# Performance work log

Measured on AMD Instinct MI355X. Metric: run time of the kernel, lower is better.

Reference implementation:

```python
import jax, jax.numpy as jnp
import numpy as np
import math

T, B, C, H, W = 1, 64, 512, 8, 8
E, NH, MEM, FF = 512, 8, 32, 2048
HD = E // NH            # 64 per-head channels
TOT = HD * H * W        # 4096 = flattened per-head dim (channels x spatial)


def conv2d(x, w, b):
    # NCHW conv with 'same' padding, matching torch.nn.Conv2d(padding='same')
    y = jax.lax.conv_general_dilated(x, w, (1, 1), 'SAME',
                                     dimension_numbers=('NCHW', 'OIHW', 'NCHW'))
    return y + b[None, :, None, None]


def layernorm(x, w, b, eps=1e-5):
    # LayerNorm over (C,H,W) with elementwise affine, matching nn.LayerNorm((C,H,W))
    m = jnp.mean(x, axis=(1, 2, 3), keepdims=True)
    v = jnp.var(x, axis=(1, 2, 3), keepdims=True)
    return (x - m) * jax.lax.rsqrt(v + eps) * w[None] + b[None]


def setup_inputs() -> dict:
    key = jax.random.key(0)
    ks = jax.random.split(key, 16)
    s = 0.02
    inp = {
        'input': jax.random.normal(ks[0], (T, B, C, H, W), jnp.float32),
        'attn_mask': jax.random.randint(ks[1], (B * NH, T, MEM), 0, 2) == 1,
        'concat_k': jax.random.normal(ks[2], (B, MEM, NH, TOT), jnp.float32),
        'concat_v': jax.random.normal(ks[3], (B, MEM, NH, TOT), jnp.float32),
        'proj_w': jax.random.normal(ks[4], (3 * E, C, 3, 3), jnp.float32) * s,
        'proj_b': jnp.zeros((3 * E,), jnp.float32),
        'out_w': jax.random.normal(ks[5], (E, E, 3, 3), jnp.float32) * s,
        'out_b': jnp.zeros((E,), jnp.float32),
        'lin1_w': jax.random.normal(ks[6], (FF, E, 3, 3), jnp.float32) * s,
        'lin1_b': jnp.zeros((FF,), jnp.float32),
        'lin2_w': jax.random.normal(ks[7], (E, FF, 3, 3), jnp.float32) * s,
        'lin2_b': jnp.zeros((E,), jnp.float32),
        'n1_w': jnp.ones((E, H, W), jnp.float32),
        'n1_b': jnp.zeros((E, H, W), jnp.float32),
        'n2_w': jnp.ones((E, H, W), jnp.float32),
        'n2_b': jnp.zeros((E, H, W), jnp.float32),
        'pos_w': jax.random.normal(ks[8], (MEM, H * W * E), jnp.float32) * s,
        'pos_b': jax.random.uniform(ks[9], (MEM, NH), jnp.float32, -0.1, 0.1),
    }
    return inp


def reference(input, attn_mask, concat_k, concat_v, proj_w, proj_b, out_w, out_b,
              lin1_w, lin1_b, lin2_w, lin2_b, n1_w, n1_b, n2_w, n2_b, pos_w, pos_b):
    x = input.reshape(T * B, C, H, W)
    kqv = conv2d(x, proj_w, proj_b)                      # [B, 3E, H, W]
    k0, q0, v0 = kqv[:, :E], kqv[:, E:2 * E], kqv[:, 2 * E:]

    def split_heads(t):  # [T*B,E,H,W] -> [B*NH, T, TOT]
        return t.reshape(T, B * NH, HD, H, W).transpose(1, 0, 2, 3, 4).reshape(B * NH, T, TOT)

    k, q, v = split_heads(k0), split_heads(q0), split_heads(v0)
    q = q / math.sqrt(TOT)

    def mem_pre(c):  # [B,MEM,NH,TOT] -> [B*NH, MEM-1, TOT]
        return c[:, 1:].transpose(1, 0, 2, 3).reshape(MEM - 1, B * NH, TOT).transpose(1, 0, 2)

    k = jnp.concatenate([mem_pre(concat_k), k], axis=1)  # [B*NH, MEM, TOT]
    v = jnp.concatenate([mem_pre(concat_v), v], axis=1)

    # learned relative-position bias on keys and logits
    pw = jnp.broadcast_to(pos_w[:, None, :], (MEM, B, NH * TOT)).reshape(MEM, B * NH, TOT).transpose(1, 0, 2)
    pb = jnp.broadcast_to(pos_b[:, None, :], (MEM, B, NH)).reshape(MEM, B * NH).transpose(1, 0)
    k = k + pw

    mask = jnp.where(attn_mask, -jnp.inf, 0.0).astype(q.dtype)
    mask = mask.at[:, :, -1].set(5.0)                    # current step always attendable (+5 bias)
    logits = mask + jnp.einsum('bqd,bkd->bqk', q, k) + pb[:, None, :]
    w_attn = jax.nn.softmax(logits, axis=-1)             # [B*NH, T, MEM]
    attn = jnp.einsum('bqk,bkd->bqd', w_attn, v)         # [B*NH, T, TOT]
    attn = attn.transpose(1, 0, 2).reshape(B, E, H, W)

    out = conv2d(attn, out_w, out_b)
    ret_k = k.transpose(1, 0, 2).reshape(MEM, B, NH, TOT).transpose(1, 0, 2, 3)
    ret_v = v.transpose(1, 0, 2).reshape(MEM, B, NH, TOT).transpose(1, 0, 2, 3)

    # norm_first=False path
    out = out + x[:, :E]
    out = layernorm(out, n1_w, n1_b)
    ff = conv2d(jax.nn.relu(conv2d(out, lin1_w, lin1_b)), lin2_w, lin2_b)
    out = layernorm(out + ff, n2_w, n2_b)
    return (out[None], ret_k, ret_v)
```

## Files before the change

kernel.cpp:

```cpp
#include <hip/hip_runtime.h>
#include <hip/hip_bf16.h>
#include <stdint.h>

typedef __attribute__((ext_vector_type(8))) short bf16x8;
typedef __attribute__((ext_vector_type(4))) float f32x4;

static __device__ __forceinline__ unsigned short f2bf(float f) {
  union { float f; unsigned int u; } v; v.f = f;
  unsigned int u = v.u;
  return (unsigned short)((u + 0x7FFFu + ((u >> 16) & 1u)) >> 16);
}

static __device__ __forceinline__ void gld16(const void* g, void* l) {
  __builtin_amdgcn_global_load_lds(
      (const __attribute__((address_space(1))) unsigned int*)g,
      (__attribute__((address_space(3))) unsigned int*)l, 16, 0, 0);
}

__global__ __launch_bounds__(256) void k_zero(uint4* __restrict__ p, int n) {
  int i = blockIdx.x * 256 + threadIdx.x;
  if (i < n) p[i] = make_uint4(0u, 0u, 0u, 0u);
}

__global__ __launch_bounds__(256) void k_wcvt(const float* __restrict__ in,
                                              unsigned short* __restrict__ out, int C) {
  int o = blockIdx.x, c0 = blockIdx.y << 9;
  int t = threadIdx.x;
  __shared__ float l[4608];
  const float* src = in + ((size_t)o * C + c0) * 9;
  for (int j = t; j < 4608; j += 256) l[j] = src[j];
  __syncthreads();
  unsigned short* dst = out + (size_t)o * 9 * C;
#pragma unroll
  for (int j = 0; j < 18; ++j) {
    int f = t * 18 + j;
    int tap = f >> 9, c = f & 511;
    dst[(size_t)tap * C + c0 + c] = f2bf(l[c * 9 + tap]);
  }
}

__global__ __launch_bounds__(256) void k_x2pad(const float* __restrict__ x,
                                               unsigned short* __restrict__ xp) {
  int b = blockIdx.x >> 3, c0 = (blockIdx.x & 7) << 6;
  int t = threadIdx.x;
  __shared__ float l[64][65];
  int cr = t >> 2, p0 = (t & 3) << 4;
  const float* src = x + ((size_t)b * 512 + c0 + cr) * 64 + p0;
#pragma unroll
  for (int j = 0; j < 4; ++j) {
    float4 v = *(const float4*)(src + j * 4);
    l[cr][p0 + j * 4 + 0] = v.x; l[cr][p0 + j * 4 + 1] = v.y;
    l[cr][p0 + j * 4 + 2] = v.z; l[cr][p0 + j * 4 + 3] = v.w;
  }
  __syncthreads();
  int pix = t >> 2, cc0 = (t & 3) << 4;
  size_t prow = (size_t)b * 100 + 11 + (pix >> 3) * 10 + (pix & 7);
  unsigned short pk[16];
#pragma unroll
  for (int j = 0; j < 16; ++j) pk[j] = f2bf(l[cc0 + j][pix]);
  *(uint4*)(xp + prow * 512 + c0 + cc0) = *(const uint4*)pk;
  *(uint4*)(xp + prow * 512 + c0 + cc0 + 8) = *(const uint4*)(pk + 8);
}

template <int EPI>
__global__ __launch_bounds__(256, 2) void k_gemm9(
    const unsigned short* __restrict__ Wt, int ldK,
    const unsigned short* __restrict__ Xp, int C, int tlog,
    int kiter, const float* __restrict__ bias,
    void* __restrict__ outv, int Cout, size_t zstride) {
  __shared__ unsigned short lds[2][2][8192];
  int t = threadIdx.x, lane = t & 63, wid = t >> 6;
  int O0 = blockIdx.x << 7, M0 = blockIdx.y << 7;
  int kbase = blockIdx.z * kiter;
  int srow = lane >> 3, skg = (lane & 7) << 3;

  int wrow[4], pbv[4];
#pragma unroll
  for (int i = 0; i < 4; ++i) {
    int rl = wid * 8 + i * 32 + srow;
    wrow[i] = O0 + rl;
    int m = M0 + rl, b = m >> 6, pix = m & 63;
    pbv[i] = b * 100 + (pix >> 3) * 10 + (pix & 7);
  }

  f32x4 acc[4][4];
#pragma unroll
  for (int i = 0; i < 4; ++i)
#pragma unroll
    for (int j = 0; j < 4; ++j) acc[i][j] = (f32x4){0.f, 0.f, 0.f, 0.f};

  auto stage = [&](int buf, int kt) {
    int gk = kbase + kt;
    int tap = gk >> tlog;
    int c0 = (gk - (tap << tlog)) << 6;
    int toff = tap + 7 * ((tap * 11) >> 5);
#pragma unroll
    for (int i = 0; i < 4; ++i) {
      gld16(Wt + (size_t)wrow[i] * ldK + (gk << 6) + skg,
            &lds[buf][0][(wid * 8 + i * 32) * 64]);
      gld16(Xp + (size_t)(pbv[i] + toff) * C + c0 + skg,
            &lds[buf][1][(wid * 8 + i * 32) * 64]);
    }
  };

  int wr = wid >> 1, wc = wid & 1;
  int frow = lane & 15, fkb = (lane >> 4) << 3;

  auto compute = [&](int buf) {
    const unsigned short* Wl = &lds[buf][0][0];
    const unsigned short* Xl = &lds[buf][1][0];
#pragma unroll
    for (int kk = 0; kk < 2; ++kk) {
      bf16x8 af[4], bfv[4];
#pragma unroll
      for (int f = 0; f < 4; ++f) {
        af[f]  = *(const bf16x8*)(Wl + ((wr * 64 + f * 16 + frow) << 6) + kk * 32 + fkb);
        bfv[f] = *(const bf16x8*)(Xl + ((wc * 64 + f * 16 + frow) << 6) + kk * 32 + fkb);
      }
#pragma unroll
      for (int fi = 0; fi < 4; ++fi)
#pragma unroll
        for (int fj = 0; fj < 4; ++fj)
          acc[fi][fj] = __builtin_amdgcn_mfma_f32_16x16x32_bf16(af[fi], bfv[fj], acc[fi][fj], 0, 0, 0);
    }
  };

  stage(0, 0);
  __syncthreads();
  for (int kt = 0; kt < kiter; ++kt) {
    int cur = kt & 1;
    if (kt + 1 < kiter) stage(cur ^ 1, kt + 1);
    compute(cur);
    __syncthreads();
  }

  int ob = O0 + wr * 64, mb = M0 + wc * 64;
  int r0 = (lane >> 4) << 2, cm = lane & 15;
  if (EPI == 4) {
    unsigned short* outp = (unsigned short*)outv;
#pragma unroll
    for (int fi = 0; fi < 4; ++fi) {
      int oo = ob + fi * 16 + r0;
      float4 bv = *(const float4*)(bias + oo);
#pragma unroll
      for (int fj = 0; fj < 4; ++fj) {
        int mm = mb + fj * 16 + cm;
        int bb = mm >> 6, pix = mm & 63;
        size_t prow = (size_t)bb * 100 + 11 + (pix >> 3) * 10 + (pix & 7);
        unsigned short pk[4];
        pk[0] = f2bf(fmaxf(acc[fi][fj][0] + bv.x, 0.f));
        pk[1] = f2bf(fmaxf(acc[fi][fj][1] + bv.y, 0.f));
        pk[2] = f2bf(fmaxf(acc[fi][fj][2] + bv.z, 0.f));
        pk[3] = f2bf(fmaxf(acc[fi][fj][3] + bv.w, 0.f));
        *(ushort4*)(outp + prow * Cout + oo) = *(const ushort4*)pk;
      }
    }
  } else {
    float* out = (float*)outv + (size_t)blockIdx.z * zstride;
#pragma unroll
    for (int fi = 0; fi < 4; ++fi) {
#pragma unroll
      for (int fj = 0; fj < 4; ++fj) {
        int mm = mb + fj * 16 + cm;
        int bb = mm >> 6, pix = mm & 63;
#pragma unroll
        for (int r = 0; r < 4; ++r) {
          int oo = ob + fi * 16 + r0 + r;
          float v = acc[fi][fj][r];
          if (EPI == 0) v += bias[oo];
          out[((size_t)bb * Cout + oo) * 64 + pix] = v;
        }
      }
    }
  }
}

__global__ __launch_bounds__(256) void k_attnK(
    const float* __restrict__ kqv, const float* __restrict__ ck,
    const float* __restrict__ pw, const float* __restrict__ pb,
    float* __restrict__ rk, float* __restrict__ logits) {
  int idx = blockIdx.x;
  int h = idx & 7, m = (idx >> 3) & 31, b = idx >> 8;
  int t = threadIdx.x, lane = t & 63, wid = t >> 6;
  int i0 = t << 4;
  int hd = i0 >> 6, pix = i0 & 63;

  const float* src = (m < 31)
      ? (ck + (((size_t)(b * 32 + m + 1) * 8 + h) << 12) + i0)
      : (kqv + ((size_t)(b * 1536 + h * 64 + hd) << 6) + pix);
  const float* qs = kqv + ((size_t)(b * 1536 + 512 + h * 64 + hd) << 6) + pix;
  const float* pws = pw + ((size_t)m << 15) + (h << 12) + i0;
  float* dst = rk + (((size_t)(b * 32 + m) * 8 + h) << 12) + i0;

  float part = 0.f;
#pragma unroll
  for (int j = 0; j < 4; ++j) {
    float4 a = *(const float4*)(src + j * 4);
    float4 p = *(const float4*)(pws + j * 4);
    float4 q = *(const float4*)(qs + j * 4);
    float4 kk;
    kk.x = a.x + p.x; kk.y = a.y + p.y; kk.z = a.z + p.z; kk.w = a.w + p.w;
    *(float4*)(dst + j * 4) = kk;
    part += 0.015625f * (q.x * kk.x + q.y * kk.y + q.z * kk.z + q.w * kk.w);
  }
#pragma unroll
  for (int s = 32; s; s >>= 1) part += __shfl_xor(part, s);
  __shared__ float red[4];
  if (lane == 0) red[wid] = part;
  __syncthreads();
  if (t == 0)
    logits[((b << 3) + h) * 32 + m] = red[0] + red[1] + red[2] + red[3] + pb[m * 8 + h];
}

__global__ __launch_bounds__(256) void k_attnV(
    const float* __restrict__ kqv, const int* __restrict__ mask,
    const float* __restrict__ cv, const float* __restrict__ logits,
    float* __restrict__ rv, float* __restrict__ attnb) {
  int bh = blockIdx.x, b = bh >> 3, h = bh & 7;
  int t = threadIdx.x;
  int d = (blockIdx.y << 10) + (t << 2);
  int hd = d >> 6, pix = d & 63;

  float lg[32];
#pragma unroll
  for (int j = 0; j < 8; ++j) {
    float4 v = *(const float4*)(logits + bh * 32 + j * 4);
    lg[j * 4 + 0] = v.x; lg[j * 4 + 1] = v.y; lg[j * 4 + 2] = v.z; lg[j * 4 + 3] = v.w;
  }
  float mx = -INFINITY;
#pragma unroll
  for (int m = 0; m < 32; ++m) {
    if (m == 31) lg[m] += 5.0f;
    else if (mask[bh * 32 + m] != 0) lg[m] = -INFINITY;
    mx = fmaxf(mx, lg[m]);
  }
  float sm = 0.f;
#pragma unroll
  for (int m = 0; m < 32; ++m) { lg[m] = __expf(lg[m] - mx); sm += lg[m]; }
  float rs = 1.f / sm;

  float4 acc = make_float4(0.f, 0.f, 0.f, 0.f);
  for (int m = 0; m < 32; ++m) {
    const float* src = (m < 31)
        ? (cv + (((size_t)(b * 32 + m + 1) * 8 + h) << 12) + d)
        : (kqv + ((size_t)(b * 1536 + 1024 + h * 64 + hd) << 6) + pix);
    float4 v = *(const float4*)src;
    *(float4*)(rv + (((size_t)(b * 32 + m) * 8 + h) << 12) + d) = v;
    float wm = lg[m] * rs;
    acc.x += wm * v.x; acc.y += wm * v.y; acc.z += wm * v.z; acc.w += wm * v.w;
  }
  *(float4*)(attnb + ((size_t)(b * 512 + h * 64 + hd) << 6) + pix) = acc;
}

__global__ __launch_bounds__(256) void k_lnfuse(
    const float* __restrict__ a, const float* __restrict__ b,
    const float* __restrict__ resid, const float* __restrict__ bias,
    const float* __restrict__ w, const float* __restrict__ beta,
    float* __restrict__ out) {
  int bb = blockIdx.x, t = threadIdx.x, lane = t & 63, wid = t >> 6;
  size_t base = (size_t)bb << 15;
  float s = 0.f, sq = 0.f;
  for (int i = t * 4; i < 32768; i += 1024) {
    float4 va = *(const float4*)(a + base + i);
    float4 vb = *(const float4*)(b + base + i);
    float4 vr = *(const float4*)(resid + base + i);
    float bs = bias[i >> 6];
    float x0 = va.x + vb.x + vr.x + bs, x1 = va.y + vb.y + vr.y + bs;
    float x2 = va.z + vb.z + vr.z + bs, x3 = va.w + vb.w + vr.w + bs;
    s += x0 + x1 + x2 + x3;
    sq += x0 * x0 + x1 * x1 + x2 * x2 + x3 * x3;
  }
#pragma unroll
  for (int k = 32; k; k >>= 1) { s += __shfl_xor(s, k); sq += __shfl_xor(sq, k); }
  __shared__ float rsm[4], rqm[4];
  if (lane == 0) { rsm[wid] = s; rqm[wid] = sq; }
  __syncthreads();
  s = rsm[0] + rsm[1] + rsm[2] + rsm[3];
  sq = rqm[0] + rqm[1] + rqm[2] + rqm[3];
  float mean = s * (1.f / 32768.f);
  float var = sq * (1.f / 32768.f) - mean * mean;
  float rinv = rsqrtf(var + 1e-5f);
  for (int i = t * 4; i < 32768; i += 1024) {
    float4 va = *(const float4*)(a + base + i);
    float4 vb = *(const float4*)(b + base + i);
    float4 vr = *(const float4*)(resid + base + i);
    float bs = bias[i >> 6];
    float4 vw = *(const float4*)(w + i);
    float4 vt = *(const float4*)(beta + i);
    float4 r;
    r.x = (va.x + vb.x + vr.x + bs - mean) * rinv * vw.x + vt.x;
    r.y = (va.y + vb.y + vr.y + bs - mean) * rinv * vw.y + vt.y;
    r.z = (va.z + vb.z + vr.z + bs - mean) * rinv * vw.z + vt.z;
    r.w = (va.w + vb.w + vr.w + bs - mean) * rinv * vw.w + vt.w;
    *(float4*)(out + base + i) = r;
  }
}

extern "C" void kernel_launch(void* const* d_in, const int* in_sizes, int n_in,
                              void* d_out, int out_size, void* d_ws, size_t ws_size,
                              hipStream_t stream) {
  const float* x     = (const float*)d_in[0];
  const int*   mask  = (const int*)d_in[1];
  const float* ck    = (const float*)d_in[2];
  const float* cv    = (const float*)d_in[3];
  const float* projw = (const float*)d_in[4];
  const float* projb = (const float*)d_in[5];
  const float* outw  = (const float*)d_in[6];
  const float* outb  = (const float*)d_in[7];
  const float* l1w   = (const float*)d_in[8];
  const float* l1b   = (const float*)d_in[9];
  const float* l2w   = (const float*)d_in[10];
  const float* l2b   = (const float*)d_in[11];
  const float* n1w   = (const float*)d_in[12];
  const float* n1b   = (const float*)d_in[13];
  const float* n2w   = (const float*)d_in[14];
  const float* n2b   = (const float*)d_in[15];
  const float* posw  = (const float*)d_in[16];
  const float* posb  = (const float*)d_in[17];

  char* ws = (char*)d_ws;
  unsigned short* wbP   = (unsigned short*)(ws);
  unsigned short* wbO   = (unsigned short*)(ws + 14155776);
  unsigned short* wbL1  = (unsigned short*)(ws + 18874368);
  unsigned short* wbL2  = (unsigned short*)(ws + 37748736);
  unsigned short* xpadI = (unsigned short*)(ws + 56623104);
  unsigned short* apad  = (unsigned short*)(ws + 63176704);
  unsigned short* l1pad = (unsigned short*)(ws + 69730304);
  unsigned short* ffpad = (unsigned short*)(ws + 76283904);
  float* kqv    = (float*)(ws + 102498304);
  float* logits = (float*)(ws + 127664128);
  float* res_a  = (float*)(ws + 127729664);
  float* res_b  = (float*)(ws + 136118272);
  float* ln1    = (float*)(ws + 144506880);
  float* attnb  = (float*)(ws + 152895488);

  float* out0 = (float*)d_out;
  float* rk = out0 + 2097152;
  float* rv = rk + 67108864;

  k_zero<<<11200, 256, 0, stream>>>((uint4*)(ws + 56623104), 2867200);

  k_wcvt<<<dim3(1536, 1), 256, 0, stream>>>(projw, wbP, 512);
  k_wcvt<<<dim3(512, 1), 256, 0, stream>>>(outw, wbO, 512);
  k_wcvt<<<dim3(2048, 1), 256, 0, stream>>>(l1w, wbL1, 512);
  k_wcvt<<<dim3(512, 4), 256, 0, stream>>>(l2w, wbL2, 2048);

  k_x2pad<<<512, 256, 0, stream>>>(x, xpadI);

  k_gemm9<0><<<dim3(12, 32, 1), 256, 0, stream>>>(wbP, 4608, xpadI, 512, 3, 72, projb, kqv, 1536, 0);

  k_attnK<<<16384, 256, 0, stream>>>(kqv, ck, posw, posb, rk, logits);
  k_attnV<<<dim3(512, 4), 256, 0, stream>>>(kqv, mask, cv, logits, rv, attnb);
  k_x2pad<<<512, 256, 0, stream>>>(attnb, apad);

  k_gemm9<3><<<dim3(4, 32, 2), 256, 0, stream>>>(wbO, 4608, apad, 512, 3, 36, nullptr, res_a, 512, 2097152);
  k_lnfuse<<<64, 256, 0, stream>>>(res_a, res_b, x, outb, n1w, n1b, ln1);
  k_x2pad<<<512, 256, 0, stream>>>(ln1, l1pad);

  k_gemm9<4><<<dim3(16, 32, 1), 256, 0, stream>>>(wbL1, 4608, l1pad, 512, 3, 72, l1b, ffpad, 2048, 0);

  k_gemm9<3><<<dim3(4, 32, 2), 256, 0, stream>>>(wbL2, 18432, ffpad, 2048, 5, 144, nullptr, res_a, 512, 2097152);
  k_lnfuse<<<64, 256, 0, stream>>>(res_a, res_b, ln1, l2b, n2w, n2b, out0);
}
```

Before: 891.4 us.

## Increase split-K for conv GEMMs and remap block indices across XCDs

```diff
diff --git a/kernel.cpp b/kernel.cpp
--- a/kernel.cpp
+++ b/kernel.cpp
@@ -70,7 +70,14 @@
     void* __restrict__ outv, int Cout, size_t zstride) {
   __shared__ unsigned short lds[2][2][8192];
   int t = threadIdx.x, lane = t & 63, wid = t >> 6;
-  int O0 = blockIdx.x << 7, M0 = blockIdx.y << 7;
+
+  int gx = gridDim.x;
+  int f = blockIdx.x + blockIdx.y * gx;
+  int cpx = (gx * gridDim.y) >> 3;
+  int fs = (f & 7) * cpx + (f >> 3);
+  int bx = fs % gx, by = fs / gx;
+
+  int O0 = bx << 7, M0 = by << 7;
   int kbase = blockIdx.z * kiter;
   int srow = lane >> 3, skg = (lane & 7) << 3;
 
@@ -113,9 +120,9 @@
     for (int kk = 0; kk < 2; ++kk) {
       bf16x8 af[4], bfv[4];
 #pragma unroll
-      for (int f = 0; f < 4; ++f) {
-        af[f]  = *(const bf16x8*)(Wl + ((wr * 64 + f * 16 + frow) << 6) + kk * 32 + fkb);
-        bfv[f] = *(const bf16x8*)(Xl + ((wc * 64 + f * 16 + frow) << 6) + kk * 32 + fkb);
+      for (int ff = 0; ff < 4; ++ff) {
+        af[ff]  = *(const bf16x8*)(Wl + ((wr * 64 + ff * 16 + frow) << 6) + kk * 32 + fkb);
+        bfv[ff] = *(const bf16x8*)(Xl + ((wc * 64 + ff * 16 + frow) << 6) + kk * 32 + fkb);
       }
 #pragma unroll
       for (int fi = 0; fi < 4; ++fi)
@@ -175,6 +182,19 @@
   }
 }
 
+__global__ __launch_bounds__(256) void k_sum2(const float* __restrict__ a,
+                                              const float* __restrict__ b,
+                                              const float* __restrict__ bias,
+                                              float* __restrict__ o) {
+  int i = (blockIdx.x * 256 + threadIdx.x) * 4;
+  int ch = (i >> 6) % 1536;
+  float4 va = *(const float4*)(a + i);
+  float4 vb = *(const float4*)(b + i);
+  float bs = bias[ch];
+  *(float4*)(o + i) = make_float4(va.x + vb.x + bs, va.y + vb.y + bs,
+                                  va.z + vb.z + bs, va.w + vb.w + bs);
+}
+
 __global__ __launch_bounds__(256) void k_attnK(
     const float* __restrict__ kqv, const float* __restrict__ ck,
     const float* __restrict__ pw, const float* __restrict__ pb,
@@ -252,8 +272,9 @@
   *(float4*)(attnb + ((size_t)(b * 512 + h * 64 + hd) << 6) + pix) = acc;
 }
 
-__global__ __launch_bounds__(256) void k_lnfuse(
-    const float* __restrict__ a, const float* __restrict__ b,
+__global__ __launch_bounds__(256) void k_lnfuse4(
+    const float* __restrict__ p0, const float* __restrict__ p1,
+    const float* __restrict__ p2, const float* __restrict__ p3,
     const float* __restrict__ resid, const float* __restrict__ bias,
     const float* __restrict__ w, const float* __restrict__ beta,
     float* __restrict__ out) {
@@ -261,12 +282,16 @@
   size_t base = (size_t)bb << 15;
   float s = 0.f, sq = 0.f;
   for (int i = t * 4; i < 32768; i += 1024) {
-    float4 va = *(const float4*)(a + base + i);
-    float4 vb = *(const float4*)(b + base + i);
+    float4 v0 = *(const float4*)(p0 + base + i);
+    float4 v1 = *(const float4*)(p1 + base + i);
+    float4 v2 = *(const float4*)(p2 + base + i);
+    float4 v3 = *(const float4*)(p3 + base + i);
     float4 vr = *(const float4*)(resid + base + i);
     float bs = bias[i >> 6];
-    float x0 = va.x + vb.x + vr.x + bs, x1 = va.y + vb.y + vr.y + bs;
-    float x2 = va.z + vb.z + vr.z + bs, x3 = va.w + vb.w + vr.w + bs;
+    float x0 = v0.x + v1.x + v2.x + v3.x + vr.x + bs;
+    float x1 = v0.y + v1.y + v2.y + v3.y + vr.y + bs;
+    float x2 = v0.z + v1.z + v2.z + v3.z + vr.z + bs;
+    float x3 = v0.w + v1.w + v2.w + v3.w + vr.w + bs;
     s += x0 + x1 + x2 + x3;
     sq += x0 * x0 + x1 * x1 + x2 * x2 + x3 * x3;
   }
@@ -281,17 +306,19 @@
   float var = sq * (1.f / 32768.f) - mean * mean;
   float rinv = rsqrtf(var + 1e-5f);
   for (int i = t * 4; i < 32768; i += 1024) {
-    float4 va = *(const float4*)(a + base + i);
-    float4 vb = *(const float4*)(b + base + i);
+    float4 v0 = *(const float4*)(p0 + base + i);
+    float4 v1 = *(const float4*)(p1 + base + i);
+    float4 v2 = *(const float4*)(p2 + base + i);
+    float4 v3 = *(const float4*)(p3 + base + i);
     float4 vr = *(const float4*)(resid + base + i);
     float bs = bias[i >> 6];
     float4 vw = *(const float4*)(w + i);
     float4 vt = *(const float4*)(beta + i);
     float4 r;
-    r.x = (va.x + vb.x + vr.x + bs - mean) * rinv * vw.x + vt.x;
-    r.y = (va.y + vb.y + vr.y + bs - mean) * rinv * vw.y + vt.y;
-    r.z = (va.z + vb.z + vr.z + bs - mean) * rinv * vw.z + vt.z;
-    r.w = (va.w + vb.w + vr.w + bs - mean) * rinv * vw.w + vt.w;
+    r.x = (v0.x + v1.x + v2.x + v3.x + vr.x + bs - mean) * rinv * vw.x + vt.x;
+    r.y = (v0.y + v1.y + v2.y + v3.y + vr.y + bs - mean) * rinv * vw.y + vt.y;
+    r.z = (v0.z + v1.z + v2.z + v3.z + vr.z + bs - mean) * rinv * vw.z + vt.z;
+    r.w = (v0.w + v1.w + v2.w + v3.w + vr.w + bs - mean) * rinv * vw.w + vt.w;
     *(float4*)(out + base + i) = r;
   }
 }
@@ -327,12 +354,13 @@
   unsigned short* apad  = (unsigned short*)(ws + 63176704);
   unsigned short* l1pad = (unsigned short*)(ws + 69730304);
   unsigned short* ffpad = (unsigned short*)(ws + 76283904);
-  float* kqv    = (float*)(ws + 102498304);
-  float* logits = (float*)(ws + 127664128);
-  float* res_a  = (float*)(ws + 127729664);
-  float* res_b  = (float*)(ws + 136118272);
-  float* ln1    = (float*)(ws + 144506880);
-  float* attnb  = (float*)(ws + 152895488);
+  float* kqvA   = (float*)(ws + 102498304);
+  float* kqvB   = (float*)(ws + 127664128);
+  float* kqv    = (float*)(ws + 152829952);
+  float* logits = (float*)(ws + 177995776);
+  float* res    = (float*)(ws + 178061312);
+  float* ln1    = (float*)(ws + 211615744);
+  float* attnb  = (float*)(ws + 220004352);
 
   float* out0 = (float*)d_out;
   float* rk = out0 + 2097152;
@@ -347,18 +375,21 @@
 
   k_x2pad<<<512, 256, 0, stream>>>(x, xpadI);
 
-  k_gemm9<0><<<dim3(12, 32, 1), 256, 0, stream>>>(wbP, 4608, xpadI, 512, 3, 72, projb, kqv, 1536, 0);
+  k_gemm9<3><<<dim3(12, 32, 2), 256, 0, stream>>>(wbP, 4608, xpadI, 512, 3, 36, nullptr, kqvA, 1536, 25165824 / 4);
+  k_sum2<<<6144, 256, 0, stream>>>(kqvA, kqvB, projb, kqv);
 
   k_attnK<<<16384, 256, 0, stream>>>(kqv, ck, posw, posb, rk, logits);
   k_attnV<<<dim3(512, 4), 256, 0, stream>>>(kqv, mask, cv, logits, rv, attnb);
   k_x2pad<<<512, 256, 0, stream>>>(attnb, apad);
 
-  k_gemm9<3><<<dim3(4, 32, 2), 256, 0, stream>>>(wbO, 4608, apad, 512, 3, 36, nullptr, res_a, 512, 2097152);
-  k_lnfuse<<<64, 256, 0, stream>>>(res_a, res_b, x, outb, n1w, n1b, ln1);
+  k_gemm9<3><<<dim3(4, 32, 4), 256, 0, stream>>>(wbO, 4608, apad, 512, 3, 18, nullptr, res, 512, 2097152);
+  k_lnfuse4<<<64, 256, 0, stream>>>(res, res + 2097152, res + 4194304, res + 6291456,
+                                    x, outb, n1w, n1b, ln1);
   k_x2pad<<<512, 256, 0, stream>>>(ln1, l1pad);
 
   k_gemm9<4><<<dim3(16, 32, 1), 256, 0, stream>>>(wbL1, 4608, l1pad, 512, 3, 72, l1b, ffpad, 2048, 0);
 
-  k_gemm9<3><<<dim3(4, 32, 2), 256, 0, stream>>>(wbL2, 18432, ffpad, 2048, 5, 144, nullptr, res_a, 512, 2097152);
-  k_lnfuse<<<64, 256, 0, stream>>>(res_a, res_b, ln1, l2b, n2w, n2b, out0);
-}
+  k_gemm9<3><<<dim3(4, 32, 4), 256, 0, stream>>>(wbL2, 18432, ffpad, 2048, 5, 72, nullptr, res, 512, 2097152);
+  k_lnfuse4<<<64, 256, 0, stream>>>(res, res + 2097152, res + 4194304, res + 6291456,
+                                    ln1, l2b, n2w, n2b, out0);
+}
```

Measured after the change: 845.9 us. 5.1% less time.
